# Performance work log

Hardware: AMD Instinct MI355X
Metric: run time of the kernel (lower is better)

The kernel has to match this reference:

```python
import jax, jax.numpy as jnp
import numpy as np

HIDDEN = 2048
NUM_HEADS = 6
HEAD_V = 512          # head_dim * expand_v = 256 * 2
VALUE_DIM = NUM_HEADS * HEAD_V  # 3072
CONV_K = 4
PHASE_BASE = 10000.0
EPS = 1e-5


def _causal_depthwise_conv(x, w):
    # x: [B, T, C], w: [C, K]; causal depthwise conv, no bias, no activation
    B, T, C = x.shape
    K = w.shape[1]
    xp = jnp.pad(x, ((0, 0), (K - 1, 0), (0, 0)))
    y = jnp.zeros_like(x)
    for j in range(K):
        y = y + xp[:, j:j + T, :] * w[:, j]
    return y


def _rotate(x, ang):
    # x: [..., D] interleaved RoPE pairs, ang: [..., D//2] pair angles
    cos = jnp.cos(ang)
    sin = jnp.sin(ang)
    xe = x[..., ::2]
    xo = x[..., 1::2]
    ye = xe * cos - xo * sin
    yo = xo * cos + xe * sin
    return jnp.stack([ye, yo], axis=-1).reshape(x.shape)


def setup_inputs() -> dict:
    key = jax.random.key(0)
    ks = jax.random.split(key, 12)
    s = 0.02
    return {
        "hidden_states": jax.random.normal(ks[0], (2, 2048, HIDDEN), jnp.float32),
        "Wq": jax.random.normal(ks[1], (HIDDEN, VALUE_DIM), jnp.float32) * s,
        "Wk": jax.random.normal(ks[2], (HIDDEN, VALUE_DIM), jnp.float32) * s,
        "Wv": jax.random.normal(ks[3], (HIDDEN, VALUE_DIM), jnp.float32) * s,
        "Wa": jax.random.normal(ks[4], (HIDDEN, NUM_HEADS), jnp.float32) * s,
        "Wb": jax.random.normal(ks[5], (HIDDEN, NUM_HEADS), jnp.float32) * s,
        "Wg": jax.random.normal(ks[6], (HIDDEN, VALUE_DIM), jnp.float32) * s,
        "Wo": jax.random.normal(ks[7], (VALUE_DIM, HIDDEN), jnp.float32) * s,
        "conv_q": jax.random.normal(ks[8], (VALUE_DIM, CONV_K), jnp.float32) * s,
        "conv_k": jax.random.normal(ks[9], (VALUE_DIM, CONV_K), jnp.float32) * s,
        "conv_v": jax.random.normal(ks[10], (VALUE_DIM, CONV_K), jnp.float32) * s,
        "rms_w": jnp.ones((HEAD_V,), jnp.float32),
    }


def _forward(hidden_states, Wq, Wk, Wv, Wa, Wb, Wg, Wo, conv_q, conv_k, conv_v, rms_w):
    B, T, _ = hidden_states.shape
    H, D = NUM_HEADS, HEAD_V
    inv_freq = 1.0 / (PHASE_BASE ** (jnp.arange(0, D, 2, dtype=jnp.float32) / D))  # [D/2]

    q = _causal_depthwise_conv(hidden_states @ Wq, conv_q).reshape(B, T, H, D)
    k = _causal_depthwise_conv(hidden_states @ Wk, conv_k).reshape(B, T, H, D)
    v = _causal_depthwise_conv(hidden_states @ Wv, conv_v).reshape(B, T, H, D)

    # pair angles (RoPE-style): raw even channels scaled by inverse frequencies
    theta = q[..., ::2] * inv_freq           # [B, T, H, D/2] output/query phase
    psi = k[..., ::2] * inv_freq             # write phase
    # state rotation per step = phase increment so cumulative state phase tracks theta
    phi = theta - jnp.concatenate([jnp.zeros_like(theta[:, :1]), theta[:, :-1]], axis=1)

    alpha = jax.nn.sigmoid(hidden_states @ Wa)  # [B, T, H] decay gate
    beta = jax.nn.sigmoid(hidden_states @ Wb)   # [B, T, H] write gate

    # time-major scan inputs
    tm = lambda a: jnp.moveaxis(a, 1, 0)
    xs = (tm(theta), tm(psi), tm(phi), tm(v), tm(alpha), tm(beta))

    def step(state, inp):
        th, ps, ph, vt, at, bt = inp  # state: [B, H, D]
        retained = _rotate(state, ph) * at[..., None]
        write = _rotate(vt, ps)
        new_state = retained + bt[..., None] * write
        out_t = _rotate(new_state, -th)
        return new_state, out_t

    state0 = jnp.zeros((B, H, D), hidden_states.dtype)
    _, out = jax.lax.scan(step, state0, xs)     # out: [T, B, H, D]
    out = jnp.moveaxis(out, 0, 1)               # [B, T, H, D]

    # gated RMSNorm over head_v_dim, then output projection
    g = (hidden_states @ Wg).reshape(B, T, H, D)
    rms = jax.lax.rsqrt(jnp.mean(jnp.square(out), axis=-1, keepdims=True) + EPS)
    o = out * rms * rms_w * jax.nn.silu(g)
    return (o.reshape(B, T, VALUE_DIM) @ Wo)


def reference(hidden_states, Wq, Wk, Wv, Wa, Wb, Wg, Wo, conv_q, conv_k, conv_v, rms_w):
    return _forward(hidden_states, Wq, Wk, Wv, Wa, Wb, Wg, Wo, conv_q, conv_k, conv_v, rms_w)
```

## Files before the change

kernel.cpp:

```cpp
#include <hip/hip_runtime.h>
#include <hip/hip_bf16.h>
#include <stdint.h>

using bf16 = __hip_bfloat16;
using mfrag = __attribute__((ext_vector_type(8))) __bf16;
using f32x4 = __attribute__((ext_vector_type(4))) float;

#define TOKENS 4096
#define HID    2048
#define VD     3072
#define NH     6
#define HD     512
#define NPAIR  256
#define N1     9216
#define NC     128
#define CHUNK  16

#define NPREP1 ((N1 / 32) * (HID / 32))
#define NPREP2 ((HID / 32) * (VD / 32))

__device__ __forceinline__ void gld_lds16(const bf16* g, bf16* l) {
    __builtin_amdgcn_global_load_lds((const __attribute__((address_space(1))) void*)g,
                                     (__attribute__((address_space(3))) void*)l, 16, 0, 0);
}

#define VMWAIT(n) asm volatile("s_waitcnt vmcnt(" #n ")" ::: "memory")
#define SCHED0    __builtin_amdgcn_sched_barrier(0)
#define SBAR      __builtin_amdgcn_s_barrier()

template<int BN_T>
__device__ __forceinline__ void gemm_body(int bid, const bf16* __restrict__ A,
                                          const bf16* __restrict__ Bt,
                                          void* __restrict__ Cv,
                                          int M, int N, int K, int obf,
                                          int n0, int nbn, char* smem) {
    constexpr int WN   = (BN_T == 256) ? 4 : 2;
    constexpr int WM   = 8 / WN;
    constexpr int MF   = (256 / WM) / 16;
    constexpr int AQ   = MF / 4;
    constexpr int SH   = AQ * 16;
    constexpr int NHT  = 2 + BN_T / 128;
    constexpr int HT   = 16384;
    constexpr int SLOT = NHT * HT;

    const int tid  = threadIdx.x;
    const int wave = tid >> 6;
    const int lane = tid & 63;
    const int lrow = lane & 15;
    const int lk   = lane >> 4;
    const int wm   = wave / WN;
    const int wn   = wave % WN;

    const int xcd = bid & 7;
    const int kk2 = bid >> 3;
    const int rn  = nbn >> 1;
    const int jj  = kk2 & 31;
    const int bm  = ((((xcd >> 1) << 2) + (jj & 3)) << 8);
    const int bn  = ((xcd & 1) * rn + (kk2 >> 5) * 8 + (jj >> 2)) * BN_T;

    const int NT = K >> 6;

    auto ST_B = [&](int half, int t) {
        char* sb = smem + (size_t)(t & 1) * SLOT + (2 + half) * HT;
        const int ko = t << 6;
#pragma unroll
        for (int i = 0; i < 2; ++i) {
            const int L = i * 512 + tid;
            const int r = L >> 3;
            const int c = (L & 7) ^ (r & 7);
            gld_lds16(Bt + (size_t)(bn + half * 128 + r) * K + ko + c * 8,
                      (bf16*)(sb + (size_t)L * 16));
        }
    };
    auto ST_A = [&](int unit, int t) {
        char* sb = smem + (size_t)(t & 1) * SLOT;
        const int ko = t << 6;
        const int s  = tid / (SH * 8);
        const int W  = tid % (SH * 8);
        const int rl = W >> 3;
        const int c  = W & 7;
        const int r256 = s * (256 / WM) + unit * SH + rl;
        const int cl = c ^ (r256 & 7);
        const int ht = r256 >> 7, lr = r256 & 127;
        gld_lds16(A + (size_t)(bm + r256) * K + ko + cl * 8,
                  (bf16*)(sb + (size_t)ht * HT + (size_t)lr * 128 + c * 16));
    };

    auto rdA = [&](const char* rb, int mf, int kk) -> mfrag {
        const int r  = wm * (MF * 16) + mf * 16 + lrow;
        const int ht = r >> 7, lr = r & 127;
        const int cc = (kk * 4 + lk) ^ (lr & 7);
        return *(const mfrag*)(rb + (size_t)ht * HT + (size_t)lr * 128 + cc * 16);
    };
    auto rdB = [&](const char* rb, int nf, int kk) -> mfrag {
        const int r  = wn * 64 + nf * 16 + lrow;
        const int ht = r >> 7, lr = r & 127;
        const int cc = (kk * 4 + lk) ^ (lr & 7);
        return *(const mfrag*)(rb + (size_t)(2 + ht) * HT + (size_t)lr * 128 + cc * 16);
    };

    f32x4 acc[MF][4];
#pragma unroll
    for (int m = 0; m < MF; ++m)
#pragma unroll
        for (int n = 0; n < 4; ++n) acc[m][n] = f32x4{0.f, 0.f, 0.f, 0.f};

    ST_B(0, 0);
    if (BN_T == 256) ST_B(1, 0);
    ST_A(0, 0); ST_A(1, 0); ST_A(2, 0); ST_A(3, 0);

#define RD_A(AF, band)                                                          \
    _Pragma("unroll")                                                           \
    for (int i = 0; i < AQ; ++i)                                                \
        _Pragma("unroll")                                                       \
        for (int kx = 0; kx < 2; ++kx) AF[i][kx] = rdA(rb, (band) * AQ + i, kx);

#define MFMA_Q(q, AF)                                                           \
    __builtin_amdgcn_s_setprio(1);                                              \
    _Pragma("unroll")                                                           \
    for (int i = 0; i < AQ; ++i)                                                \
        _Pragma("unroll")                                                       \
        for (int nf = 0; nf < 4; ++nf) {                                        \
            const int mi = (q) * AQ + i;                                        \
            acc[mi][nf] = __builtin_amdgcn_mfma_f32_16x16x32_bf16(AF[i][0], bfr[nf][0], acc[mi][nf], 0, 0, 0); \
            acc[mi][nf] = __builtin_amdgcn_mfma_f32_16x16x32_bf16(AF[i][1], bfr[nf][1], acc[mi][nf], 0, 0, 0); \
        }                                                                       \
    __builtin_amdgcn_s_setprio(0);

    if constexpr (BN_T == 128) {
        for (int kt = 0; kt < NT; ++kt) {
            const char* rb = smem + (size_t)(kt & 1) * SLOT;
            const bool last = (kt == NT - 1);
            mfrag bfr[4][2];
            mfrag afA[2][2], afB[2][2];

            VMWAIT(2);
            SCHED0; SBAR;
#pragma unroll
            for (int nf = 0; nf < 4; ++nf)
#pragma unroll
                for (int kx = 0; kx < 2; ++kx) bfr[nf][kx] = rdB(rb, nf, kx);
#pragma unroll
            for (int i = 0; i < 2; ++i)
#pragma unroll
                for (int kx = 0; kx < 2; ++kx) afA[i][kx] = rdA(rb, i, kx);
            if (!last) { ST_B(0, kt + 1); ST_A(0, kt + 1); ST_A(1, kt + 1); }
            SCHED0;
            __builtin_amdgcn_s_setprio(1);
#pragma unroll
            for (int i = 0; i < 2; ++i)
#pragma unroll
                for (int nf = 0; nf < 4; ++nf) {
                    acc[i][nf] = __builtin_amdgcn_mfma_f32_16x16x32_bf16(afA[i][0], bfr[nf][0], acc[i][nf], 0, 0, 0);
                    acc[i][nf] = __builtin_amdgcn_mfma_f32_16x16x32_bf16(afA[i][1], bfr[nf][1], acc[i][nf], 0, 0, 0);
                }
            __builtin_amdgcn_s_setprio(0);

            if (last) { VMWAIT(0); } else { VMWAIT(4); }
            SCHED0; SBAR;
#pragma unroll
            for (int i = 0; i < 2; ++i)
#pragma unroll
                for (int kx = 0; kx < 2; ++kx) afB[i][kx] = rdA(rb, 2 + i, kx);
            if (!last) { ST_A(2, kt + 1); ST_A(3, kt + 1); }
            SCHED0;
            __builtin_amdgcn_s_setprio(1);
#pragma unroll
            for (int i = 0; i < 2; ++i)
#pragma unroll
                for (int nf = 0; nf < 4; ++nf) {
                    acc[2 + i][nf] = __builtin_amdgcn_mfma_f32_16x16x32_bf16(afB[i][0], bfr[nf][0], acc[2 + i][nf], 0, 0, 0);
                    acc[2 + i][nf] = __builtin_amdgcn_mfma_f32_16x16x32_bf16(afB[i][1], bfr[nf][1], acc[2 + i][nf], 0, 0, 0);
                }
            __builtin_amdgcn_s_setprio(0);
        }
    } else {
        for (int kt = 0; kt < NT; ++kt) {
            const char* rb = smem + (size_t)(kt & 1) * SLOT;
            const bool last = (kt == NT - 1);
            mfrag bfr[4][2];
            mfrag af0[AQ][2], af1[AQ][2], af2[AQ][2], af3[AQ][2];

            VMWAIT(2);
            SCHED0; SBAR;
#pragma unroll
            for (int nf = 0; nf < 4; ++nf)
#pragma unroll
                for (int kx = 0; kx < 2; ++kx) bfr[nf][kx] = rdB(rb, nf, kx);
            RD_A(af0, 0)
            if (!last) ST_B(0, kt + 1);
            RD_A(af1, 1)
            SCHED0;
            MFMA_Q(0, af0)

            if (last) { VMWAIT(1); } else { VMWAIT(3); }
            SCHED0; SBAR;
            if (!last) ST_B(1, kt + 1);
            RD_A(af2, 2)
            SCHED0;
            MFMA_Q(1, af1)

            if (last) { VMWAIT(0); } else { VMWAIT(4); }
            SCHED0; SBAR;
            if (!last) { ST_A(0, kt + 1); ST_A(1, kt + 1); }
            RD_A(af3, 3)
            SCHED0;
            MFMA_Q(2, af2)

            SBAR;
            if (!last) { ST_A(2, kt + 1); ST_A(3, kt + 1); }
            SCHED0;
            MFMA_Q(3, af3)
        }
    }
#undef RD_A
#undef MFMA_Q

#pragma unroll
    for (int m = 0; m < MF; ++m)
#pragma unroll
        for (int j2 = 0; j2 < 4; ++j2) {
            const int r = bm + wm * (MF * 16) + m * 16 + lk * 4 + j2;
#pragma unroll
            for (int n = 0; n < 4; ++n) {
                const int c = n0 + bn + wn * 64 + n * 16 + lrow;
                if (obf) ((bf16*)Cv)[(size_t)r * N + c] = __float2bfloat16(acc[m][n][j2]);
                else     ((float*)Cv)[(size_t)r * N + c] = acc[m][n][j2];
            }
        }
}

__global__ __launch_bounds__(512, 2) void k_gemm1(const bf16* __restrict__ A,
                                                  const bf16* __restrict__ Wt,
                                                  bf16* __restrict__ X) {
    extern __shared__ char smem[];
    if (blockIdx.x < 512)
        gemm_body<256>(blockIdx.x, A, Wt, X, TOKENS, N1, HID, 1, 0, 32, smem);
    else
        gemm_body<128>(blockIdx.x - 512, A, Wt + (size_t)8192 * HID, X, TOKENS, N1, HID, 1, 8192, 8, smem);
}

__global__ __launch_bounds__(512, 2) void k_gemm2k(const bf16* __restrict__ A,
                                                   const bf16* __restrict__ Bt,
                                                   float* __restrict__ C) {
    extern __shared__ char smem[];
    gemm_body<128>(blockIdx.x, A, Bt, C, TOKENS, HID, VD, 0, 0, 16, smem);
}

__global__ __launch_bounds__(256) void k_front(const float* __restrict__ hs,
                                               const float* __restrict__ Wq, const float* __restrict__ Wk,
                                               const float* __restrict__ Wv, const float* __restrict__ Wg,
                                               const float* __restrict__ Wo,
                                               const float* __restrict__ Wa, const float* __restrict__ Wb,
                                               bf16* __restrict__ Wt, bf16* __restrict__ Wot,
                                               float* __restrict__ alpha, float* __restrict__ beta,
                                               bf16* __restrict__ hsb) {
    const int bid = blockIdx.x;
    const int tid = threadIdx.x;
    __shared__ float t[32][33];
    __shared__ float red[12][4];

    if (bid < NPREP1) {
        const int tx = tid & 31, ty = tid >> 5;
        const int n0 = (bid % (N1 / 32)) * 32;
        const int k0 = (bid / (N1 / 32)) * 32;
        const float* src; int cb, cs;
        if (n0 < 1536)      { int m = n0;        src = Wq; cb = (m >> 8) * 512 + (m & 255) * 2; cs = 2; }
        else if (n0 < 3072) { int m = n0 - 1536; src = Wk; cb = (m >> 8) * 512 + (m & 255) * 2; cs = 2; }
        else if (n0 < 6144) { int m = n0 - 3072; src = Wv; cb = m; cs = 1; }
        else                { int m = n0 - 6144; src = Wg; cb = m; cs = 1; }
#pragma unroll
        for (int i = 0; i < 4; ++i) {
            int k = k0 + ty + i * 8;
            t[ty + i * 8][tx] = src[(size_t)k * VD + cb + cs * tx];
        }
        __syncthreads();
#pragma unroll
        for (int i = 0; i < 4; ++i) {
            int n = n0 + ty + i * 8;
            Wt[(size_t)n * HID + k0 + tx] = __float2bfloat16(t[tx][ty + i * 8]);
        }
    } else if (bid < NPREP1 + NPREP2) {
        const int b2 = bid - NPREP1;
        const int tx = tid & 31, ty = tid >> 5;
        const int c0 = (b2 % (HID / 32)) * 32;
        const int r0 = (b2 / (HID / 32)) * 32;
#pragma unroll
        for (int i = 0; i < 4; ++i)
            t[ty + i * 8][tx] = Wo[(size_t)(r0 + ty + i * 8) * HID + c0 + tx];
        __syncthreads();
#pragma unroll
        for (int i = 0; i < 4; ++i)
            Wot[(size_t)(c0 + ty + i * 8) * VD + r0 + tx] = __float2bfloat16(t[tx][ty + i * 8]);
    } else {
        const int tok = bid - NPREP1 - NPREP2;
        const float* hrow = hs + (size_t)tok * HID;
        bf16* hbrow = hsb + (size_t)tok * HID;
        const int k0 = tid * 8;
        float4 h1 = *(const float4*)(hrow + k0);
        float4 h2 = *(const float4*)(hrow + k0 + 4);
        float hv[8] = {h1.x, h1.y, h1.z, h1.w, h2.x, h2.y, h2.z, h2.w};
        {
            __hip_bfloat162 pr[4];
#pragma unroll
            for (int i = 0; i < 4; ++i) {
                pr[i].x = __float2bfloat16(hv[2 * i]);
                pr[i].y = __float2bfloat16(hv[2 * i + 1]);
            }
            *(uint4*)(hbrow + k0) = *(const uint4*)pr;
        }
        float part[12];
#pragma unroll
        for (int j = 0; j < 12; ++j) part[j] = 0.f;
#pragma unroll
        for (int i = 0; i < 8; ++i) {
            const int k = k0 + i;
            float2 a0 = *(const float2*)(Wa + (size_t)k * NH);
            float2 a1 = *(const float2*)(Wa + (size_t)k * NH + 2);
            float2 a2 = *(const float2*)(Wa + (size_t)k * NH + 4);
            float2 b0 = *(const float2*)(Wb + (size_t)k * NH);
            float2 b1 = *(const float2*)(Wb + (size_t)k * NH + 2);
            float2 b2 = *(const float2*)(Wb + (size_t)k * NH + 4);
            const float x = hv[i];
            part[0]  = fmaf(x, a0.x, part[0]);  part[1]  = fmaf(x, a0.y, part[1]);
            part[2]  = fmaf(x, a1.x, part[2]);  part[3]  = fmaf(x, a1.y, part[3]);
            part[4]  = fmaf(x, a2.x, part[4]);  part[5]  = fmaf(x, a2.y, part[5]);
            part[6]  = fmaf(x, b0.x, part[6]);  part[7]  = fmaf(x, b0.y, part[7]);
            part[8]  = fmaf(x, b1.x, part[8]);  part[9]  = fmaf(x, b1.y, part[9]);
            part[10] = fmaf(x, b2.x, part[10]); part[11] = fmaf(x, b2.y, part[11]);
        }
        const int lane = tid & 63, wv = tid >> 6;
#pragma unroll
        for (int j = 0; j < 12; ++j) {
            float s = part[j];
            for (int off = 32; off; off >>= 1) s += __shfl_down(s, off);
            if (lane == 0) red[j][wv] = s;
        }
        __syncthreads();
        if (tid < 12) {
            float s = red[tid][0] + red[tid][1] + red[tid][2] + red[tid][3];
            float v = 1.f / (1.f + expf(-s));
            if (tid < 6) alpha[(size_t)tok * NH + tid] = v;
            else         beta [(size_t)tok * NH + tid - 6] = v;
        }
    }
}

__global__ __launch_bounds__(256) void k_scan1(const bf16* __restrict__ X,
                                               const float* __restrict__ alpha,
                                               const float* __restrict__ beta,
                                               const float* __restrict__ cq,
                                               const float* __restrict__ ck,
                                               const float* __restrict__ cv,
                                               bf16* __restrict__ U, float* __restrict__ pp) {
    const int bx = blockIdx.x;
    const int c  = bx % NC;
    const int h  = (bx / NC) % NH;
    const int b  = bx / (NC * NH);
    const int p  = threadIdx.x;
    const int t0 = c * CHUNK;
    const int ch2 = h * HD + 2 * p;
    const float wq0 = cq[ch2 * 4 + 0], wq1 = cq[ch2 * 4 + 1], wq2 = cq[ch2 * 4 + 2], wq3 = cq[ch2 * 4 + 3];
    const float wk0 = ck[ch2 * 4 + 0], wk1 = ck[ch2 * 4 + 1], wk2 = ck[ch2 * 4 + 2], wk3 = ck[ch2 * 4 + 3];
    const float wa0 = cv[ch2 * 4 + 0], wa1 = cv[ch2 * 4 + 1], wa2 = cv[ch2 * 4 + 2], wa3 = cv[ch2 * 4 + 3];
    const float wb0 = cv[(ch2 + 1) * 4 + 0], wb1 = cv[(ch2 + 1) * 4 + 1],
                wb2 = cv[(ch2 + 1) * 4 + 2], wb3 = cv[(ch2 + 1) * 4 + 3];
    const float invf = exp2f(-13.287712379549449f * ((float)p * (1.0f / 256.0f)));
    const int qcol = h * NPAIR + p;
    const int kcol = 1536 + h * NPAIR + p;
    const int vcol = 3072 + ch2;

    float xq[3], xk[3], xv0[3], xv1[3];
#pragma unroll
    for (int i = 0; i < 3; ++i) {
        int t = t0 - 3 + i;
        if (t >= 0) {
            size_t tok = (size_t)b * 2048 + t;
            const bf16* xr = X + tok * N1;
            xq[i] = __bfloat162float(xr[qcol]);
            xk[i] = __bfloat162float(xr[kcol]);
            __hip_bfloat162 vv = *(const __hip_bfloat162*)&xr[vcol];
            xv0[i] = __bfloat162float(vv.x);
            xv1[i] = __bfloat162float(vv.y);
        } else { xq[i] = xk[i] = xv0[i] = xv1[i] = 0.f; }
    }

    float u0 = 0.f, u1 = 0.f, ap = 1.f;
#pragma unroll 4
    for (int t = t0; t < t0 + CHUNK; ++t) {
        const size_t tok = (size_t)b * 2048 + t;
        const bf16* xr = X + tok * N1;
        float nq = __bfloat162float(xr[qcol]);
        float nk = __bfloat162float(xr[kcol]);
        __hip_bfloat162 vv = *(const __hip_bfloat162*)&xr[vcol];
        float nv0 = __bfloat162float(vv.x);
        float nv1 = __bfloat162float(vv.y);
        float yq  = wq3 * nq  + wq2 * xq[2]  + wq1 * xq[1]  + wq0 * xq[0];
        float yk  = wk3 * nk  + wk2 * xk[2]  + wk1 * xk[1]  + wk0 * xk[0];
        float yv0 = wa3 * nv0 + wa2 * xv0[2] + wa1 * xv0[1] + wa0 * xv0[0];
        float yv1 = wb3 * nv1 + wb2 * xv1[2] + wb1 * xv1[1] + wb0 * xv1[0];
        xq[0] = xq[1]; xq[1] = xq[2]; xq[2] = nq;
        xk[0] = xk[1]; xk[1] = xk[2]; xk[2] = nk;
        xv0[0] = xv0[1]; xv0[1] = xv0[2]; xv0[2] = nv0;
        xv1[0] = xv1[1]; xv1[1] = xv1[2]; xv1[2] = nv1;
        float theta = yq * invf, psi = yk * invf;
        float d = psi - theta, sn, cs;
        __sincosf(d, &sn, &cs);
        float w0 = yv0 * cs - yv1 * sn;
        float w1 = yv1 * cs + yv0 * sn;
        float a  = alpha[tok * NH + h];
        float bb = beta [tok * NH + h];
        u0 = fmaf(a, u0, bb * w0);
        u1 = fmaf(a, u1, bb * w1);
        ap *= a;
        __hip_bfloat162 us;
        us.x = __float2bfloat16(u0);
        us.y = __float2bfloat16(u1);
        *(__hip_bfloat162*)&U[tok * (size_t)VD + h * HD + 2 * p] = us;
        if (p == 0) pp[tok * NH + h] = ap;
    }
}

__global__ __launch_bounds__(512) void k_carry(const bf16* __restrict__ U, const float* __restrict__ pp,
                                               float* __restrict__ carry) {
    const int bh = blockIdx.x;
    const int b = bh / NH, h = bh % NH;
    const int d = threadIdx.x;
    float s = 0.f;
    for (int cb = 0; cb < NC; cb += 32) {
        float ue[32], pv[32];
#pragma unroll
        for (int i = 0; i < 32; ++i) {
            size_t tok = (size_t)b * 2048 + (cb + i) * CHUNK + CHUNK - 1;
            ue[i] = __bfloat162float(U[tok * (size_t)VD + h * HD + d]);
            pv[i] = pp[tok * NH + h];
        }
#pragma unroll
        for (int i = 0; i < 32; ++i) {
            carry[((size_t)bh * NC + cb + i) * HD + d] = s;
            s = ue[i] + pv[i] * s;
        }
    }
}

__global__ __launch_bounds__(256) void k_pass3(const bf16* __restrict__ U, const float* __restrict__ pp,
                                               const float* __restrict__ carry, const bf16* __restrict__ X,
                                               const float* __restrict__ rms_w, bf16* __restrict__ O) {
    const int r    = blockIdx.x * 4 + (threadIdx.x >> 6);
    const int lane = threadIdx.x & 63;
    const size_t tok = r / NH;
    const int h = r % NH;
    const int b = (int)(tok >> 11);
    const int t = (int)(tok & 2047);
    const int c = t / CHUNK;
    const size_t ubase = tok * (size_t)VD + h * HD;
    const size_t cbase = ((size_t)(b * NH + h) * NC + c) * HD;
    const float P = pp[tok * NH + h];

    float u0v[4], u1v[4];
    float s = 0.f;
#pragma unroll
    for (int i = 0; i < 4; ++i) {
        const int pi = lane + i * 64;
        __hip_bfloat162 uu = *(const __hip_bfloat162*)&U[ubase + 2 * pi];
        float2 cy = *(const float2*)&carry[cbase + 2 * pi];
        float u0 = fmaf(P, cy.x, __bfloat162float(uu.x));
        float u1 = fmaf(P, cy.y, __bfloat162float(uu.y));
        u0v[i] = u0; u1v[i] = u1;
        s = fmaf(u0, u0, s);
        s = fmaf(u1, u1, s);
    }
#pragma unroll
    for (int off = 32; off; off >>= 1) s += __shfl_xor(s, off);
    const float rms = rsqrtf(s * (1.f / 512.f) + 1e-5f);

#pragma unroll
    for (int i = 0; i < 4; ++i) {
        const int pi = lane + i * 64;
        __hip_bfloat162 gg = *(const __hip_bfloat162*)&X[tok * N1 + 6144 + h * HD + 2 * pi];
        float g0 = __bfloat162float(gg.x), g1 = __bfloat162float(gg.y);
        float si0 = g0 / (1.f + expf(-g0));
        float si1 = g1 / (1.f + expf(-g1));
        float2 rw = *(const float2*)&rms_w[2 * pi];
        __hip_bfloat162 ob;
        ob.x = __float2bfloat16(u0v[i] * rms * rw.x * si0);
        ob.y = __float2bfloat16(u1v[i] * rms * rw.y * si1);
        *(__hip_bfloat162*)&O[ubase + 2 * pi] = ob;
    }
}

extern "C" void kernel_launch(void* const* d_in, const int* in_sizes, int n_in,
                              void* d_out, int out_size, void* d_ws, size_t ws_size,
                              hipStream_t stream) {
    const float* hs   = (const float*)d_in[0];
    const float* Wq   = (const float*)d_in[1];
    const float* Wk   = (const float*)d_in[2];
    const float* Wv   = (const float*)d_in[3];
    const float* Wa   = (const float*)d_in[4];
    const float* Wb   = (const float*)d_in[5];
    const float* Wg   = (const float*)d_in[6];
    const float* Wo   = (const float*)d_in[7];
    const float* cq   = (const float*)d_in[8];
    const float* ck   = (const float*)d_in[9];
    const float* cv   = (const float*)d_in[10];
    const float* rmsw = (const float*)d_in[11];

    char* ws = (char*)d_ws;
    size_t off = 0;
    auto alloc = [&](size_t bytes) -> void* {
        void* p = ws + off;
        off = (off + bytes + 255) & ~(size_t)255;
        return p;
    };
    bf16*  hsb   = (bf16*) alloc((size_t)TOKENS * HID * 2);
    bf16*  Wt    = (bf16*) alloc((size_t)N1 * HID * 2);
    bf16*  Wot   = (bf16*) alloc((size_t)HID * VD * 2);
    bf16*  X     = (bf16*) alloc((size_t)TOKENS * N1 * 2);
    bf16*  U     = (bf16*) alloc((size_t)TOKENS * VD * 2);
    float* alp   = (float*)alloc((size_t)TOKENS * NH * 4);
    float* bet   = (float*)alloc((size_t)TOKENS * NH * 4);
    float* pp    = (float*)alloc((size_t)TOKENS * NH * 4);
    float* carry = (float*)alloc((size_t)2 * NH * NC * HD * 4);
    bf16*  O     = (bf16*)Wt;

    hipFuncSetAttribute((const void*)k_gemm1,
                        hipFuncAttributeMaxDynamicSharedMemorySize, 2 * 4 * 16384);
    hipFuncSetAttribute((const void*)k_gemm2k,
                        hipFuncAttributeMaxDynamicSharedMemorySize, 2 * 3 * 16384);

    k_front<<<dim3(NPREP1 + NPREP2 + TOKENS), 256, 0, stream>>>(
        hs, Wq, Wk, Wv, Wg, Wo, Wa, Wb, Wt, Wot, alp, bet, hsb);
    k_gemm1<<<dim3(640), 512, 2 * 4 * 16384, stream>>>(hsb, Wt, X);
    k_scan1<<<2 * NH * NC, 256, 0, stream>>>(X, alp, bet, cq, ck, cv, U, pp);
    k_carry<<<2 * NH, 512, 0, stream>>>(U, pp, carry);
    k_pass3<<<TOKENS * NH / 4, 256, 0, stream>>>(U, pp, carry, X, rmsw, O);
    k_gemm2k<<<dim3(256), 512, 2 * 3 * 16384, stream>>>(O, Wot, (float*)d_out);
}
```

Before: 315.3 us.

## Use 256x128 tiles with BK=32 for the first projection GEMM at higher occupancy

Replaces the first fused projection GEMM's mixed 256x256/256x128 tiles with a new 256x128 tile body that steps K by 32, using 48KB of LDS double-buffering and launch bounds of 4 blocks per CU. The grid grows to 1152 blocks. The goal is more resident blocks per CU so latency is hidden and the tail is better balanced. The cost is half as many MFMAs per barrier, twice as many K iterations, and no XOR swizzle on the new 64-byte LDS rows, which may cause bank conflicts. The generic gemm_body is reduced to its 128-wide path only.

```diff
diff --git a/kernel.cpp b/kernel.cpp
--- a/kernel.cpp
+++ b/kernel.cpp
@@ -28,18 +28,135 @@
 #define SCHED0    __builtin_amdgcn_sched_barrier(0)
 #define SBAR      __builtin_amdgcn_s_barrier()
 
+__device__ __forceinline__ void gemm_body32(int bid, const bf16* __restrict__ A,
+                                            const bf16* __restrict__ Bt,
+                                            void* __restrict__ Cv,
+                                            int N, int K, int obf,
+                                            int n0, int nbn, char* smem) {
+    constexpr int SLOT = 24576;
+    const int tid  = threadIdx.x;
+    const int wave = tid >> 6;
+    const int lane = tid & 63;
+    const int lrow = lane & 15;
+    const int lk   = lane >> 4;
+    const int wm   = wave >> 1;
+    const int wn   = wave & 1;
+
+    const int xcd = bid & 7;
+    const int kk2 = bid >> 3;
+    const int rn  = nbn >> 1;
+    const int jj  = kk2 & 31;
+    const int bm  = ((((xcd >> 1) << 2) + (jj & 3)) << 8);
+    const int bn  = ((xcd & 1) * rn + (kk2 >> 5) * 8 + (jj >> 2)) * 128;
+
+    const int NT = K >> 5;
+
+    auto ST_B32 = [&](int t) {
+        char* sb = smem + (size_t)(t & 1) * SLOT + 16384;
+        const int ko = t << 5;
+        const int r = tid >> 2;
+        const int c = tid & 3;
+        gld_lds16(Bt + (size_t)(bn + r) * K + ko + c * 8,
+                  (bf16*)(sb + (size_t)tid * 16));
+    };
+    auto ST_Ap = [&](int half, int t) {
+        char* sb = smem + (size_t)(t & 1) * SLOT;
+        const int ko = t << 5;
+        const int r = (tid >> 7) * 64 + ((tid >> 2) & 31) + half * 32;
+        const int c = tid & 3;
+        gld_lds16(A + (size_t)(bm + r) * K + ko + c * 8,
+                  (bf16*)(sb + (size_t)r * 64 + c * 16));
+    };
+
+    auto rdA32 = [&](const char* rb, int mf) -> mfrag {
+        const int r = wm * 64 + mf * 16 + lrow;
+        return *(const mfrag*)(rb + (size_t)r * 64 + lk * 16);
+    };
+    auto rdB32 = [&](const char* rb, int nf) -> mfrag {
+        const int r = wn * 64 + nf * 16 + lrow;
+        return *(const mfrag*)(rb + 16384 + (size_t)r * 64 + lk * 16);
+    };
+
+    f32x4 acc[4][4];
+#pragma unroll
+    for (int m = 0; m < 4; ++m)
+#pragma unroll
+        for (int n = 0; n < 4; ++n) acc[m][n] = f32x4{0.f, 0.f, 0.f, 0.f};
+
+    ST_B32(0); ST_Ap(0, 0); ST_Ap(1, 0);
+
+    for (int kt = 0; kt < NT; ++kt) {
+        const char* rb = smem + (size_t)(kt & 1) * SLOT;
+        const bool last = (kt == NT - 1);
+        mfrag bfr[4];
+        mfrag afA[2], afB[2];
+
+        VMWAIT(1);
+        SCHED0; SBAR;
+#pragma unroll
+        for (int nf = 0; nf < 4; ++nf) bfr[nf] = rdB32(rb, nf);
+        afA[0] = rdA32(rb, 0);
+        afA[1] = rdA32(rb, 1);
+        if (!last) { ST_B32(kt + 1); ST_Ap(0, kt + 1); }
+        SCHED0;
+        __builtin_amdgcn_s_setprio(1);
+#pragma unroll
+        for (int i = 0; i < 2; ++i)
+#pragma unroll
+            for (int nf = 0; nf < 4; ++nf)
+                acc[i][nf] = __builtin_amdgcn_mfma_f32_16x16x32_bf16(afA[i], bfr[nf], acc[i][nf], 0, 0, 0);
+        __builtin_amdgcn_s_setprio(0);
+
+        if (last) { VMWAIT(0); } else { VMWAIT(2); }
+        SCHED0; SBAR;
+        afB[0] = rdA32(rb, 2);
+        afB[1] = rdA32(rb, 3);
+        if (!last) ST_Ap(1, kt + 1);
+        SCHED0;
+        __builtin_amdgcn_s_setprio(1);
+#pragma unroll
+        for (int i = 0; i < 2; ++i)
+#pragma unroll
+            for (int nf = 0; nf < 4; ++nf)
+                acc[2 + i][nf] = __builtin_amdgcn_mfma_f32_16x16x32_bf16(afB[i], bfr[nf], acc[2 + i][nf], 0, 0, 0);
+        __builtin_amdgcn_s_setprio(0);
+    }
+
+#pragma unroll
+    for (int m = 0; m < 4; ++m)
+#pragma unroll
+        for (int j2 = 0; j2 < 4; ++j2) {
+            const int r = bm + wm * 64 + m * 16 + lk * 4 + j2;
+#pragma unroll
+            for (int n = 0; n < 4; ++n) {
+                const int c = n0 + bn + wn * 64 + n * 16 + lrow;
+                if (obf) ((bf16*)Cv)[(size_t)r * N + c] = __float2bfloat16(acc[m][n][j2]);
+                else     ((float*)Cv)[(size_t)r * N + c] = acc[m][n][j2];
+            }
+        }
+}
+
+__global__ __launch_bounds__(512, 4) void k_gemm1(const bf16* __restrict__ A,
+                                                  const bf16* __restrict__ Wt,
+                                                  bf16* __restrict__ X) {
+    extern __shared__ char smem[];
+    if (blockIdx.x < 1024)
+        gemm_body32(blockIdx.x, A, Wt, X, N1, HID, 1, 0, 64, smem);
+    else
+        gemm_body32(blockIdx.x - 1024, A, Wt + (size_t)8192 * HID, X, N1, HID, 1, 8192, 8, smem);
+}
+
 template<int BN_T>
 __device__ __forceinline__ void gemm_body(int bid, const bf16* __restrict__ A,
                                           const bf16* __restrict__ Bt,
                                           void* __restrict__ Cv,
                                           int M, int N, int K, int obf,
                                           int n0, int nbn, char* smem) {
-    constexpr int WN   = (BN_T == 256) ? 4 : 2;
+    constexpr int WN   = 2;
     constexpr int WM   = 8 / WN;
     constexpr int MF   = (256 / WM) / 16;
-    constexpr int AQ   = MF / 4;
-    constexpr int SH   = AQ * 16;
-    constexpr int NHT  = 2 + BN_T / 128;
+    constexpr int SH   = (MF / 4) * 16;
+    constexpr int NHT  = 3;
     constexpr int HT   = 16384;
     constexpr int SLOT = NHT * HT;
 
@@ -106,115 +223,54 @@
         for (int n = 0; n < 4; ++n) acc[m][n] = f32x4{0.f, 0.f, 0.f, 0.f};
 
     ST_B(0, 0);
-    if (BN_T == 256) ST_B(1, 0);
     ST_A(0, 0); ST_A(1, 0); ST_A(2, 0); ST_A(3, 0);
 
-#define RD_A(AF, band)                                                          \
-    _Pragma("unroll")                                                           \
-    for (int i = 0; i < AQ; ++i)                                                \
-        _Pragma("unroll")                                                       \
-        for (int kx = 0; kx < 2; ++kx) AF[i][kx] = rdA(rb, (band) * AQ + i, kx);
-
-#define MFMA_Q(q, AF)                                                           \
-    __builtin_amdgcn_s_setprio(1);                                              \
-    _Pragma("unroll")                                                           \
-    for (int i = 0; i < AQ; ++i)                                                \
-        _Pragma("unroll")                                                       \
-        for (int nf = 0; nf < 4; ++nf) {                                        \
-            const int mi = (q) * AQ + i;                                        \
-            acc[mi][nf] = __builtin_amdgcn_mfma_f32_16x16x32_bf16(AF[i][0], bfr[nf][0], acc[mi][nf], 0, 0, 0); \
-            acc[mi][nf] = __builtin_amdgcn_mfma_f32_16x16x32_bf16(AF[i][1], bfr[nf][1], acc[mi][nf], 0, 0, 0); \
-        }                                                                       \
-    __builtin_amdgcn_s_setprio(0);
-
-    if constexpr (BN_T == 128) {
-        for (int kt = 0; kt < NT; ++kt) {
-            const char* rb = smem + (size_t)(kt & 1) * SLOT;
-            const bool last = (kt == NT - 1);
-            mfrag bfr[4][2];
-            mfrag afA[2][2], afB[2][2];
-
-            VMWAIT(2);
-            SCHED0; SBAR;
-#pragma unroll
-            for (int nf = 0; nf < 4; ++nf)
-#pragma unroll
-                for (int kx = 0; kx < 2; ++kx) bfr[nf][kx] = rdB(rb, nf, kx);
-#pragma unroll
-            for (int i = 0; i < 2; ++i)
-#pragma unroll
-                for (int kx = 0; kx < 2; ++kx) afA[i][kx] = rdA(rb, i, kx);
-            if (!last) { ST_B(0, kt + 1); ST_A(0, kt + 1); ST_A(1, kt + 1); }
-            SCHED0;
-            __builtin_amdgcn_s_setprio(1);
-#pragma unroll
-            for (int i = 0; i < 2; ++i)
-#pragma unroll
-                for (int nf = 0; nf < 4; ++nf) {
-                    acc[i][nf] = __builtin_amdgcn_mfma_f32_16x16x32_bf16(afA[i][0], bfr[nf][0], acc[i][nf], 0, 0, 0);
-                    acc[i][nf] = __builtin_amdgcn_mfma_f32_16x16x32_bf16(afA[i][1], bfr[nf][1], acc[i][nf], 0, 0, 0);
-                }
-            __builtin_amdgcn_s_setprio(0);
-
-            if (last) { VMWAIT(0); } else { VMWAIT(4); }
-            SCHED0; SBAR;
-#pragma unroll
-            for (int i = 0; i < 2; ++i)
-#pragma unroll
-                for (int kx = 0; kx < 2; ++kx) afB[i][kx] = rdA(rb, 2 + i, kx);
-            if (!last) { ST_A(2, kt + 1); ST_A(3, kt + 1); }
-            SCHED0;
-            __builtin_amdgcn_s_setprio(1);
-#pragma unroll
-            for (int i = 0; i < 2; ++i)
-#pragma unroll
-                for (int nf = 0; nf < 4; ++nf) {
-                    acc[2 + i][nf] = __builtin_amdgcn_mfma_f32_16x16x32_bf16(afB[i][0], bfr[nf][0], acc[2 + i][nf], 0, 0, 0);
-                    acc[2 + i][nf] = __builtin_amdgcn_mfma_f32_16x16x32_bf16(afB[i][1], bfr[nf][1], acc[2 + i][nf], 0, 0, 0);
-                }
-            __builtin_amdgcn_s_setprio(0);
-        }
-    } else {
-        for (int kt = 0; kt < NT; ++kt) {
-            const char* rb = smem + (size_t)(kt & 1) * SLOT;
-            const bool last = (kt == NT - 1);
-            mfrag bfr[4][2];
-            mfrag af0[AQ][2], af1[AQ][2], af2[AQ][2], af3[AQ][2];
-
-            VMWAIT(2);
-            SCHED0; SBAR;
-#pragma unroll
-            for (int nf = 0; nf < 4; ++nf)
-#pragma unroll
-                for (int kx = 0; kx < 2; ++kx) bfr[nf][kx] = rdB(rb, nf, kx);
-            RD_A(af0, 0)
-            if (!last) ST_B(0, kt + 1);
-            RD_A(af1, 1)
-            SCHED0;
-            MFMA_Q(0, af0)
-
-            if (last) { VMWAIT(1); } else { VMWAIT(3); }
-            SCHED0; SBAR;
-            if (!last) ST_B(1, kt + 1);
-            RD_A(af2, 2)
-            SCHED0;
-            MFMA_Q(1, af1)
-
-            if (last) { VMWAIT(0); } else { VMWAIT(4); }
-            SCHED0; SBAR;
-            if (!last) { ST_A(0, kt + 1); ST_A(1, kt + 1); }
-            RD_A(af3, 3)
-            SCHED0;
-            MFMA_Q(2, af2)
-
-            SBAR;
-            if (!last) { ST_A(2, kt + 1); ST_A(3, kt + 1); }
-            SCHED0;
-            MFMA_Q(3, af3)
-        }
-    }
-#undef RD_A
-#undef MFMA_Q
+    for (int kt = 0; kt < NT; ++kt) {
+        const char* rb = smem + (size_t)(kt & 1) * SLOT;
+        const bool last = (kt == NT - 1);
+        mfrag bfr[4][2];
+        mfrag afA[2][2], afB[2][2];
+
+        VMWAIT(2);
+        SCHED0; SBAR;
+#pragma unroll
+        for (int nf = 0; nf < 4; ++nf)
+#pragma unroll
+            for (int kx = 0; kx < 2; ++kx) bfr[nf][kx] = rdB(rb, nf, kx);
+#pragma unroll
+        for (int i = 0; i < 2; ++i)
+#pragma unroll
+            for (int kx = 0; kx < 2; ++kx) afA[i][kx] = rdA(rb, i, kx);
+        if (!last) { ST_B(0, kt + 1); ST_A(0, kt + 1); ST_A(1, kt + 1); }
+        SCHED0;
+        __builtin_amdgcn_s_setprio(1);
+#pragma unroll
+        for (int i = 0; i < 2; ++i)
+#pragma unroll
+            for (int nf = 0; nf < 4; ++nf) {
+                acc[i][nf] = __builtin_amdgcn_mfma_f32_16x16x32_bf16(afA[i][0], bfr[nf][0], acc[i][nf], 0, 0, 0);
+                acc[i][nf] = __builtin_amdgcn_mfma_f32_16x16x32_bf16(afA[i][1], bfr[nf][1], acc[i][nf], 0, 0, 0);
+            }
+        __builtin_amdgcn_s_setprio(0);
+
+        if (last) { VMWAIT(0); } else { VMWAIT(4); }
+        SCHED0; SBAR;
+#pragma unroll
+        for (int i = 0; i < 2; ++i)
+#pragma unroll
+            for (int kx = 0; kx < 2; ++kx) afB[i][kx] = rdA(rb, 2 + i, kx);
+        if (!last) { ST_A(2, kt + 1); ST_A(3, kt + 1); }
+        SCHED0;
+        __builtin_amdgcn_s_setprio(1);
+#pragma unroll
+        for (int i = 0; i < 2; ++i)
+#pragma unroll
+            for (int nf = 0; nf < 4; ++nf) {
+                acc[2 + i][nf] = __builtin_amdgcn_mfma_f32_16x16x32_bf16(afB[i][0], bfr[nf][0], acc[2 + i][nf], 0, 0, 0);
+                acc[2 + i][nf] = __builtin_amdgcn_mfma_f32_16x16x32_bf16(afB[i][1], bfr[nf][1], acc[2 + i][nf], 0, 0, 0);
+            }
+        __builtin_amdgcn_s_setprio(0);
+    }
 
 #pragma unroll
     for (int m = 0; m < MF; ++m)
@@ -228,16 +284,6 @@
                 else     ((float*)Cv)[(size_t)r * N + c] = acc[m][n][j2];
             }
         }
-}
-
-__global__ __launch_bounds__(512, 2) void k_gemm1(const bf16* __restrict__ A,
-                                                  const bf16* __restrict__ Wt,
-                                                  bf16* __restrict__ X) {
-    extern __shared__ char smem[];
-    if (blockIdx.x < 512)
-        gemm_body<256>(blockIdx.x, A, Wt, X, TOKENS, N1, HID, 1, 0, 32, smem);
-    else
-        gemm_body<128>(blockIdx.x - 512, A, Wt + (size_t)8192 * HID, X, TOKENS, N1, HID, 1, 8192, 8, smem);
 }
 
 __global__ __launch_bounds__(512, 2) void k_gemm2k(const bf16* __restrict__ A,
@@ -524,13 +570,13 @@
     bf16*  O     = (bf16*)Wt;
 
     hipFuncSetAttribute((const void*)k_gemm1,
-                        hipFuncAttributeMaxDynamicSharedMemorySize, 2 * 4 * 16384);
+                        hipFuncAttributeMaxDynamicSharedMemorySize, 2 * 24576);
     hipFuncSetAttribute((const void*)k_gemm2k,
                         hipFuncAttributeMaxDynamicSharedMemorySize, 2 * 3 * 16384);
 
     k_front<<<dim3(NPREP1 + NPREP2 + TOKENS), 256, 0, stream>>>(
         hs, Wq, Wk, Wv, Wg, Wo, Wa, Wb, Wt, Wot, alp, bet, hsb);
-    k_gemm1<<<dim3(640), 512, 2 * 4 * 16384, stream>>>(hsb, Wt, X);
+    k_gemm1<<<dim3(1152), 512, 2 * 24576, stream>>>(hsb, Wt, X);
     k_scan1<<<2 * NH * NC, 256, 0, stream>>>(X, alp, bet, cq, ck, cv, U, pp);
     k_carry<<<2 * NH, 512, 0, stream>>>(U, pp, carry);
     k_pass3<<<TOKENS * NH / 4, 256, 0, stream>>>(U, pp, carry, X, rmsw, O);
```

Measured after the change: 339.4 us. 1.08x slower.
